# Kernel tuning notes

Hardware: AMD Instinct MI355X
Metric: run time of the kernel (lower is better)

The kernel has to match this reference:

```python
import jax, jax.numpy as jnp
import numpy as np

NUM_NODES = 20000
SEQ_LEN = 128
IN_FEATS = 2
HIDDEN = 32
N_TOTAL = NUM_NODES * SEQ_LEN  # flattened graph size
N_EDGES = 2_000_000


def setup_inputs() -> dict:
    key = jax.random.key(0)
    ks = jax.random.split(key, 10)
    x = jax.random.normal(ks[0], (NUM_NODES, SEQ_LEN, IN_FEATS), dtype=jnp.float32)
    edge_index = jax.random.randint(ks[1], (2, N_EDGES), 0, N_TOTAL, dtype=jnp.int64)
    s = 0.1
    gcn_W = jax.random.normal(ks[2], (IN_FEATS, HIDDEN), dtype=jnp.float32) * s
    gcn_b = jnp.zeros((HIDDEN,), dtype=jnp.float32)
    w_ih = jax.random.normal(ks[3], (4 * HIDDEN, HIDDEN), dtype=jnp.float32) * s
    w_hh = jax.random.normal(ks[4], (4 * HIDDEN, HIDDEN), dtype=jnp.float32) * s
    b_ih = jax.random.normal(ks[5], (4 * HIDDEN,), dtype=jnp.float32) * s
    b_hh = jax.random.normal(ks[6], (4 * HIDDEN,), dtype=jnp.float32) * s
    fc_W = jax.random.normal(ks[7], (HIDDEN, 1), dtype=jnp.float32) * s
    fc_b = jnp.zeros((1,), dtype=jnp.float32)
    return {"x": x, "edge_index": edge_index, "gcn_W": gcn_W, "gcn_b": gcn_b,
            "w_ih": w_ih, "w_hh": w_hh, "b_ih": b_ih, "b_hh": b_hh,
            "fc_W": fc_W, "fc_b": fc_b}


def _gcn(x_flat, edge_index, W, b):
    # PyG GCNConv: add self-loops, symmetric normalization, then linear+bias.
    src, dst = edge_index[0], edge_index[1]
    n = x_flat.shape[0]
    # degree at target side, including the self-loop (+1)
    deg = jax.ops.segment_sum(jnp.ones_like(dst, dtype=x_flat.dtype), dst, num_segments=n) + 1.0
    dinv = jax.lax.rsqrt(deg)  # deg >= 1 always (self-loop)
    h = x_flat @ W  # [n, HIDDEN] transform before propagate
    norm = dinv[src] * dinv[dst]  # [E]
    msg = h[src] * norm[:, None]  # gather + per-edge scale
    agg = jax.ops.segment_sum(msg, dst, num_segments=n)
    # self-loop contribution: dinv_i * dinv_i * h_i = h_i / deg_i
    out = agg + h * (1.0 / deg)[:, None]
    return out + b


def _lstm(xs, w_ih, w_hh, b_ih, b_hh):
    # torch LSTM gate order: i, f, g, o. xs: [N, S, H] -> final hidden [N, H]
    n, s, hdim = xs.shape
    xs_t = jnp.swapaxes(xs, 0, 1)  # [S, N, H]
    # precompute input projections once (dense GEMM)
    x_proj = xs_t @ w_ih.T + b_ih + b_hh  # [S, N, 4H]

    def step(carry, xp):
        h, c = carry
        g = xp + h @ w_hh.T  # [N, 4H]
        i, f, gg, o = jnp.split(g, 4, axis=-1)
        c = jax.nn.sigmoid(f) * c + jax.nn.sigmoid(i) * jnp.tanh(gg)
        h = jax.nn.sigmoid(o) * jnp.tanh(c)
        return (h, c), None

    h0 = jnp.zeros((n, hdim), dtype=xs.dtype)
    (hn, _), _ = jax.lax.scan(step, (h0, h0), x_proj)
    return hn


def reference(x, edge_index, gcn_W, gcn_b, w_ih, w_hh, b_ih, b_hh, fc_W, fc_b):
    num_nodes, seq_len, num_feats = x.shape
    x_in = x.reshape(-1, num_feats)  # [N*S, F]
    x_gcn = jax.nn.relu(_gcn(x_in, edge_index, gcn_W, gcn_b))
    x_lstm = x_gcn.reshape(num_nodes, seq_len, -1)
    hn = _lstm(x_lstm, w_ih, w_hh, b_ih, b_hh)
    return hn @ fc_W + fc_b  # [num_nodes, 1]
```

## Files before the change

kernel.cpp:

```cpp
#include <hip/hip_runtime.h>

#define SEQ 128
#define HID 32
#define TPB 128
#define XS 56

typedef __attribute__((ext_vector_type(8))) short short8;
typedef __attribute__((ext_vector_type(4))) short short4v;
typedef __attribute__((ext_vector_type(4))) float floatx4;


__global__ void count_kernel(const int* __restrict__ idx, int E, int* __restrict__ cnt) {
    int e = (blockIdx.x * blockDim.x + threadIdx.x) * 4;
    if (((E & 3) == 0) && e + 3 < E) {
        int4 d = *(const int4*)(idx + E + e);
        atomicAdd(&cnt[d.x], 1);
        atomicAdd(&cnt[d.y], 1);
        atomicAdd(&cnt[d.z], 1);
        atomicAdd(&cnt[d.w], 1);
    } else {
        int lim = min(e + 4, E);
        for (int k = e; k < lim; ++k) atomicAdd(&cnt[idx[E + k]], 1);
    }
}

__device__ __forceinline__ unsigned long long pk2(float xx, float yy, float dv) {
    int qx = __float2int_rn(xx * dv * 2097152.0f);
    int qy = __float2int_rn(yy * dv * 2097152.0f);
    return ((unsigned long long)(unsigned)(qx + (1 << 26)) << 32) |
           (unsigned)(qy + (1 << 26));
}

__global__ void scatter_pk_kernel(const int* __restrict__ idx, int E,
                                  const float2* __restrict__ x2,
                                  const int* __restrict__ deg,
                                  unsigned long long* __restrict__ aggP) {
    int e = (blockIdx.x * blockDim.x + threadIdx.x) * 4;
    if (((E & 3) == 0) && e + 3 < E) {
        int4 s = *(const int4*)(idx + e);
        int4 d = *(const int4*)(idx + E + e);
        float2 v0 = x2[s.x];
        float2 v1 = x2[s.y];
        float2 v2 = x2[s.z];
        float2 v3 = x2[s.w];
        float dv0 = rsqrtf((float)deg[s.x] + 1.0f);
        float dv1 = rsqrtf((float)deg[s.y] + 1.0f);
        float dv2 = rsqrtf((float)deg[s.z] + 1.0f);
        float dv3 = rsqrtf((float)deg[s.w] + 1.0f);
        atomicAdd(&aggP[d.x], pk2(v0.x, v0.y, dv0));
        atomicAdd(&aggP[d.y], pk2(v1.x, v1.y, dv1));
        atomicAdd(&aggP[d.z], pk2(v2.x, v2.y, dv2));
        atomicAdd(&aggP[d.w], pk2(v3.x, v3.y, dv3));
    } else {
        int lim = min(e + 4, E);
        for (int k = e; k < lim; ++k) {
            int s = idx[k];
            int d = idx[E + k];
            float2 v = x2[s];
            float dv = rsqrtf((float)deg[s] + 1.0f);
            atomicAdd(&aggP[d], pk2(v.x, v.y, dv));
        }
    }
}


__device__ __forceinline__ float sigm_f(float x) {
    return __builtin_amdgcn_rcpf(1.0f + __expf(-x));
}
__device__ __forceinline__ float tanh_f(float x) {
    return fmaf(__builtin_amdgcn_rcpf(1.0f + __expf(-2.0f * x)), 2.0f, -1.0f);
}
__device__ __forceinline__ void fsplit(float f, short& hi, short& lo) {
    unsigned u = __float_as_uint(f);
    hi = (short)(u >> 16);
    float r = f - __uint_as_float(u & 0xFFFF0000u);
    lo = (short)(__float_as_uint(r) >> 16);
}

__global__ __launch_bounds__(TPB, 2) void lstm_mfma4_kernel(
    const float2* __restrict__ x2,
    const unsigned long long* __restrict__ aggP, const int* __restrict__ deg,
    int N,
    const float* __restrict__ gcn_W, const float* __restrict__ gcn_b,
    const float* __restrict__ w_ih, const float* __restrict__ w_hh,
    const float* __restrict__ b_ih, const float* __restrict__ b_hh,
    const float* __restrict__ fc_W, const float* __restrict__ fc_b,
    float* __restrict__ out) {
    __shared__ float2 ubuf[16][SEQ + 1];
    __shared__ __align__(16) short hhb[2][16][XS];
    __shared__ __align__(16) short hlb[2][16][XS];
    __shared__ float fcp[2][16];

    const int tid = threadIdx.x;
    const int w = tid >> 6;
    const int lane = tid & 63;
    const int l15 = lane & 15;
    const int q = lane >> 4;
    const int base = blockIdx.x * 16;

    {
        const float2* xb = x2 + (size_t)base * SEQ;
        const unsigned long long* apb = aggP + (size_t)base * SEQ;
        const int* dgb = deg + (size_t)base * SEQ;
        const int lim = min(16 * SEQ, (N - base) * SEQ);
        for (int i = tid; i < 16 * SEQ; i += TPB) {
            float2 v = make_float2(0.f, 0.f);
            if (i < lim) {
                int dg = dgb[i];
                float dv = rsqrtf((float)dg + 1.0f);
                float2 xx = xb[i];
                unsigned long long pk = apb[i];
                unsigned bias = (unsigned)dg * 67108864u;
                float ax = (float)((int)((unsigned)(pk >> 32) - bias)) * (1.0f / 2097152.0f);
                float ay = (float)((int)((unsigned)pk - bias)) * (1.0f / 2097152.0f);
                v = make_float2(dv * fmaf(xx.x, dv, ax), dv * fmaf(xx.y, dv, ay));
            }
            ubuf[i >> 7][i & 127] = v;
        }
        if (tid < 16) ubuf[tid][SEQ] = make_float2(0.f, 0.f);
    }

    short8 AiH[4], AiL[4], AhH[4], AhL[4];
    floatx4 biasC[4];
    #pragma unroll
    for (int g = 0; g < 4; ++g) {
        const int arow = g * 32 + 8 * (l15 >> 2) + 4 * w + (l15 & 3);
        const float* wi = w_ih + arow * HID + 8 * q;
        const float* wh = w_hh + arow * HID + 8 * q;
        #pragma unroll
        for (int j = 0; j < 8; ++j) {
            short h16, l16;
            fsplit(wi[j], h16, l16); AiH[g][j] = h16; AiL[g][j] = l16;
            fsplit(wh[j], h16, l16); AhH[g][j] = h16; AhL[g][j] = l16;
        }
        #pragma unroll
        for (int r = 0; r < 4; ++r) {
            const int brow = g * 32 + 8 * q + 4 * w + r;
            biasC[g][r] = b_ih[brow] + b_hh[brow];
        }
    }

    float wg0[8], wg1[8], gbc[8];
    #pragma unroll
    for (int j = 0; j < 8; ++j) {
        const int u = 8 * q + j;
        wg0[j] = gcn_W[u];
        wg1[j] = gcn_W[HID + u];
        gbc[j] = gcn_b[u];
    }
    float fcw[4];
    #pragma unroll
    for (int r = 0; r < 4; ++r) fcw[r] = fc_W[8 * q + 4 * w + r];

    float c[4] = {0.f, 0.f, 0.f, 0.f};
    float ho[4] = {0.f, 0.f, 0.f, 0.f};

    __syncthreads();

#define XG_FRAGS(TT, XH, XL)                                                  \
    {                                                                         \
        float2 uu = ubuf[l15][TT];                                            \
        _Pragma("unroll") for (int j = 0; j < 8; ++j) {                       \
            float g = fmaxf(fmaf(uu.x, wg0[j], fmaf(uu.y, wg1[j], gbc[j])), 0.f); \
            short h16, l16;                                                   \
            fsplit(g, h16, l16);                                              \
            XH[j] = h16; XL[j] = l16;                                         \
        }                                                                     \
    }

    *(short4v*)&hhb[0][l15][8 * q + 4 * w] = (short4v){0, 0, 0, 0};
    *(short4v*)&hlb[0][l15][8 * q + 4 * w] = (short4v){0, 0, 0, 0};
    short8 xhA, xlA, xhB, xlB;
    floatx4 aXA[4], aXB[4];
    XG_FRAGS(0, xhA, xlA);
    #pragma unroll
    for (int g = 0; g < 4; ++g)
        aXA[g] = __builtin_amdgcn_mfma_f32_16x16x32_bf16(AiH[g], xhA, biasC[g], 0, 0, 0);
    #pragma unroll
    for (int g = 0; g < 4; ++g)
        aXA[g] = __builtin_amdgcn_mfma_f32_16x16x32_bf16(AiL[g], xhA, aXA[g], 0, 0, 0);
    #pragma unroll
    for (int g = 0; g < 4; ++g)
        aXA[g] = __builtin_amdgcn_mfma_f32_16x16x32_bf16(AiH[g], xlA, aXA[g], 0, 0, 0);
    __syncthreads();

#define LSTM_STEP(P, TT, AXC, AXN, XHN, XLN)                                               \
    do {                                                                                   \
        const short8 hh = *(const short8*)&hhb[P][l15][8 * q];                             \
        const short8 hl = *(const short8*)&hlb[P][l15][8 * q];                             \
        floatx4 acc[4];                                                                    \
        __builtin_amdgcn_s_setprio(1);                                                     \
        _Pragma("unroll") for (int g = 0; g < 4; ++g)                                      \
            acc[g] = __builtin_amdgcn_mfma_f32_16x16x32_bf16(AhH[g], hh, AXC[g], 0, 0, 0); \
        _Pragma("unroll") for (int g = 0; g < 4; ++g)                                      \
            acc[g] = __builtin_amdgcn_mfma_f32_16x16x32_bf16(AhL[g], hh, acc[g], 0, 0, 0); \
        _Pragma("unroll") for (int g = 0; g < 4; ++g)                                      \
            acc[g] = __builtin_amdgcn_mfma_f32_16x16x32_bf16(AhH[g], hl, acc[g], 0, 0, 0); \
        __builtin_amdgcn_s_setprio(0);                                                     \
        XG_FRAGS((TT) + 1, XHN, XLN);                                                      \
        __builtin_amdgcn_s_setprio(1);                                                     \
        _Pragma("unroll") for (int g = 0; g < 4; ++g)                                      \
            AXN[g] = __builtin_amdgcn_mfma_f32_16x16x32_bf16(AiH[g], XHN, biasC[g], 0, 0, 0); \
        _Pragma("unroll") for (int g = 0; g < 4; ++g)                                      \
            AXN[g] = __builtin_amdgcn_mfma_f32_16x16x32_bf16(AiL[g], XHN, AXN[g], 0, 0, 0); \
        _Pragma("unroll") for (int g = 0; g < 4; ++g)                                      \
            AXN[g] = __builtin_amdgcn_mfma_f32_16x16x32_bf16(AiH[g], XLN, AXN[g], 0, 0, 0); \
        __builtin_amdgcn_s_setprio(0);                                                     \
        {                                                                                  \
            short hi[4], lo[4];                                                            \
            _Pragma("unroll") for (int r = 0; r < 4; ++r) {                                \
                const float ig = sigm_f(acc[0][r]);                                        \
                const float fg = sigm_f(acc[1][r]);                                        \
                const float gg = tanh_f(acc[2][r]);                                        \
                const float og = sigm_f(acc[3][r]);                                        \
                c[r] = fmaf(fg, c[r], ig * gg);                                            \
                const float hv = og * tanh_f(c[r]);                                        \
                ho[r] = hv;                                                                \
                fsplit(hv, hi[r], lo[r]);                                                  \
            }                                                                              \
            *(short4v*)&hhb[(P) ^ 1][l15][8 * q + 4 * w] =                                 \
                (short4v){hi[0], hi[1], hi[2], hi[3]};                                     \
            *(short4v*)&hlb[(P) ^ 1][l15][8 * q + 4 * w] =                                 \
                (short4v){lo[0], lo[1], lo[2], lo[3]};                                     \
        }                                                                                  \
        __syncthreads();                                                                   \
    } while (0)

    #pragma unroll 1
    for (int t = 0; t < SEQ; t += 2) {
        LSTM_STEP(0, t,     aXA, aXB, xhB, xlB);
        LSTM_STEP(1, t + 1, aXB, aXA, xhA, xlA);
    }
#undef LSTM_STEP
#undef XG_FRAGS

    float partial = fmaf(ho[0], fcw[0], fmaf(ho[1], fcw[1],
                    fmaf(ho[2], fcw[2], ho[3] * fcw[3])));
    partial += __shfl_xor(partial, 16);
    partial += __shfl_xor(partial, 32);
    if (lane < 16) fcp[w][l15] = partial;
    __syncthreads();
    if (w == 0 && lane < 16) {
        const int node = base + l15;
        if (node < N) out[node] = fcp[0][l15] + fcp[1][l15] + fc_b[0];
    }
}

extern "C" void kernel_launch(void* const* d_in, const int* in_sizes, int n_in,
                              void* d_out, int out_size, void* d_ws, size_t ws_size,
                              hipStream_t stream) {
    const float* x     = (const float*)d_in[0];
    const int*   idx   = (const int*)d_in[1];
    const float* gcn_W = (const float*)d_in[2];
    const float* gcn_b = (const float*)d_in[3];
    const float* w_ih  = (const float*)d_in[4];
    const float* w_hh  = (const float*)d_in[5];
    const float* b_ih  = (const float*)d_in[6];
    const float* b_hh  = (const float*)d_in[7];
    const float* fc_W  = (const float*)d_in[8];
    const float* fc_b  = (const float*)d_in[9];

    const int num_nodes = in_sizes[0] / (SEQ * 2);
    const int ntot = num_nodes * SEQ;
    const int E = in_sizes[1] / 2;

    int* deg = (int*)d_ws;
    unsigned long long* aggP = (unsigned long long*)((char*)d_ws + (size_t)ntot * 4);

    hipMemsetAsync(d_ws, 0, (size_t)ntot * 12, stream);

    const int eb = (E + 1023) / 1024;
    count_kernel<<<eb, 256, 0, stream>>>(idx, E, deg);
    scatter_pk_kernel<<<eb, 256, 0, stream>>>(idx, E, (const float2*)x, deg, aggP);
    lstm_mfma4_kernel<<<(num_nodes + 15) / 16, TPB, 0, stream>>>(
        (const float2*)x, aggP, deg, num_nodes,
        gcn_W, gcn_b, w_ih, w_hh, b_ih, b_hh, fc_W, fc_b,
        (float*)d_out);
}
```

Before: 489.5 us.

## Run each LSTM 16-node tile in one wavefront with register-resident hidden state

The LSTM kernel moves from two waves per 16-node tile to a single 64-lane wave that computes all 32 hidden units. Weight rows are permuted so the MFMA accumulator layout matches the B-operand layout, which lets the new hidden state feed the next step straight from registers. This removes the per-timestep LDS write/read of h and the block barrier. In exchange each wave holds twice the weight fragments and accumulators and issues twice the MFMAs serially, which raises register pressure and lengthens the per-wave dependency chain.

```diff
diff --git a/kernel.cpp b/kernel.cpp
--- a/kernel.cpp
+++ b/kernel.cpp
@@ -2,11 +2,8 @@
 
 #define SEQ 128
 #define HID 32
-#define TPB 128
-#define XS 56
 
 typedef __attribute__((ext_vector_type(8))) short short8;
-typedef __attribute__((ext_vector_type(4))) short short4v;
 typedef __attribute__((ext_vector_type(4))) float floatx4;
 
 
@@ -77,7 +74,7 @@
     lo = (short)(__float_as_uint(r) >> 16);
 }
 
-__global__ __launch_bounds__(TPB, 2) void lstm_mfma4_kernel(
+__global__ __launch_bounds__(64, 1) void lstm_sw_kernel(
     const float2* __restrict__ x2,
     const unsigned long long* __restrict__ aggP, const int* __restrict__ deg,
     int N,
@@ -87,15 +84,10 @@
     const float* __restrict__ fc_W, const float* __restrict__ fc_b,
     float* __restrict__ out) {
     __shared__ float2 ubuf[16][SEQ + 1];
-    __shared__ __align__(16) short hhb[2][16][XS];
-    __shared__ __align__(16) short hlb[2][16][XS];
-    __shared__ float fcp[2][16];
-
-    const int tid = threadIdx.x;
-    const int w = tid >> 6;
-    const int lane = tid & 63;
-    const int l15 = lane & 15;
-    const int q = lane >> 4;
+
+    const int lane = threadIdx.x;
+    const int n = lane & 15;
+    const int qq = lane >> 4;
     const int base = blockIdx.x * 16;
 
     {
@@ -103,7 +95,8 @@
         const unsigned long long* apb = aggP + (size_t)base * SEQ;
         const int* dgb = deg + (size_t)base * SEQ;
         const int lim = min(16 * SEQ, (N - base) * SEQ);
-        for (int i = tid; i < 16 * SEQ; i += TPB) {
+        #pragma unroll 4
+        for (int i = lane; i < 16 * SEQ; i += 64) {
             float2 v = make_float2(0.f, 0.f);
             if (i < lim) {
                 int dg = dgb[i];
@@ -117,132 +110,154 @@
             }
             ubuf[i >> 7][i & 127] = v;
         }
-        if (tid < 16) ubuf[tid][SEQ] = make_float2(0.f, 0.f);
-    }
-
-    short8 AiH[4], AiL[4], AhH[4], AhL[4];
-    floatx4 biasC[4];
+        if (lane < 16) ubuf[lane][SEQ] = make_float2(0.f, 0.f);
+    }
+
+    short8 AiH[4][2], AiL[4][2], AhH[4][2], AhL[4][2];
+    floatx4 biasC[4][2];
     #pragma unroll
     for (int g = 0; g < 4; ++g) {
-        const int arow = g * 32 + 8 * (l15 >> 2) + 4 * w + (l15 & 3);
-        const float* wi = w_ih + arow * HID + 8 * q;
-        const float* wh = w_hh + arow * HID + 8 * q;
-        #pragma unroll
-        for (int j = 0; j < 8; ++j) {
-            short h16, l16;
-            fsplit(wi[j], h16, l16); AiH[g][j] = h16; AiL[g][j] = l16;
-            fsplit(wh[j], h16, l16); AhH[g][j] = h16; AhL[g][j] = l16;
-        }
-        #pragma unroll
-        for (int r = 0; r < 4; ++r) {
-            const int brow = g * 32 + 8 * q + 4 * w + r;
-            biasC[g][r] = b_ih[brow] + b_hh[brow];
-        }
-    }
-
-    float wg0[8], wg1[8], gbc[8];
+        #pragma unroll
+        for (int t1 = 0; t1 < 2; ++t1) {
+            const int arow = g * 32 + 8 * (n >> 2) + 4 * t1 + (n & 3);
+            const float* wi = w_ih + arow * HID + 8 * qq;
+            const float* wh = w_hh + arow * HID + 8 * qq;
+            #pragma unroll
+            for (int j = 0; j < 8; ++j) {
+                short h16, l16;
+                fsplit(wi[j], h16, l16); AiH[g][t1][j] = h16; AiL[g][t1][j] = l16;
+                fsplit(wh[j], h16, l16); AhH[g][t1][j] = h16; AhL[g][t1][j] = l16;
+            }
+            #pragma unroll
+            for (int r = 0; r < 4; ++r) {
+                const int brow = g * 32 + 8 * qq + 4 * t1 + r;
+                biasC[g][t1][r] = b_ih[brow] + b_hh[brow];
+            }
+        }
+    }
+
+    float wg0[8], wg1[8], gbc[8], fcw[8];
     #pragma unroll
     for (int j = 0; j < 8; ++j) {
-        const int u = 8 * q + j;
+        const int u = 8 * qq + j;
         wg0[j] = gcn_W[u];
         wg1[j] = gcn_W[HID + u];
         gbc[j] = gcn_b[u];
-    }
-    float fcw[4];
-    #pragma unroll
-    for (int r = 0; r < 4; ++r) fcw[r] = fc_W[8 * q + 4 * w + r];
-
-    float c[4] = {0.f, 0.f, 0.f, 0.f};
-    float ho[4] = {0.f, 0.f, 0.f, 0.f};
-
-    __syncthreads();
-
-#define XG_FRAGS(TT, XH, XL)                                                  \
-    {                                                                         \
-        float2 uu = ubuf[l15][TT];                                            \
-        _Pragma("unroll") for (int j = 0; j < 8; ++j) {                       \
-            float g = fmaxf(fmaf(uu.x, wg0[j], fmaf(uu.y, wg1[j], gbc[j])), 0.f); \
-            short h16, l16;                                                   \
-            fsplit(g, h16, l16);                                              \
-            XH[j] = h16; XL[j] = l16;                                         \
-        }                                                                     \
-    }
-
-    *(short4v*)&hhb[0][l15][8 * q + 4 * w] = (short4v){0, 0, 0, 0};
-    *(short4v*)&hlb[0][l15][8 * q + 4 * w] = (short4v){0, 0, 0, 0};
-    short8 xhA, xlA, xhB, xlB;
-    floatx4 aXA[4], aXB[4];
-    XG_FRAGS(0, xhA, xlA);
+        fcw[j] = fc_W[u];
+    }
+
+    float c[2][4], ho[2][4];
+    #pragma unroll
+    for (int t1 = 0; t1 < 2; ++t1)
+        #pragma unroll
+        for (int r = 0; r < 4; ++r) { c[t1][r] = 0.f; ho[t1][r] = 0.f; }
+
+    short8 hh = (short8){0, 0, 0, 0, 0, 0, 0, 0};
+    short8 hl = (short8){0, 0, 0, 0, 0, 0, 0, 0};
+    short8 xh, xl;
+    floatx4 aX[4][2];
+
+    {
+        float2 uu = ubuf[n][0];
+        #pragma unroll
+        for (int j = 0; j < 8; ++j) {
+            float g = fmaxf(fmaf(uu.x, wg0[j], fmaf(uu.y, wg1[j], gbc[j])), 0.f);
+            short h16, l16;
+            fsplit(g, h16, l16);
+            xh[j] = h16; xl[j] = l16;
+        }
+    }
     #pragma unroll
     for (int g = 0; g < 4; ++g)
-        aXA[g] = __builtin_amdgcn_mfma_f32_16x16x32_bf16(AiH[g], xhA, biasC[g], 0, 0, 0);
+        #pragma unroll
+        for (int t1 = 0; t1 < 2; ++t1)
+            aX[g][t1] = __builtin_amdgcn_mfma_f32_16x16x32_bf16(AiH[g][t1], xh, biasC[g][t1], 0, 0, 0);
     #pragma unroll
     for (int g = 0; g < 4; ++g)
-        aXA[g] = __builtin_amdgcn_mfma_f32_16x16x32_bf16(AiL[g], xhA, aXA[g], 0, 0, 0);
+        #pragma unroll
+        for (int t1 = 0; t1 < 2; ++t1)
+            aX[g][t1] = __builtin_amdgcn_mfma_f32_16x16x32_bf16(AiL[g][t1], xh, aX[g][t1], 0, 0, 0);
     #pragma unroll
     for (int g = 0; g < 4; ++g)
-        aXA[g] = __builtin_amdgcn_mfma_f32_16x16x32_bf16(AiH[g], xlA, aXA[g], 0, 0, 0);
-    __syncthreads();
-
-#define LSTM_STEP(P, TT, AXC, AXN, XHN, XLN)                                               \
-    do {                                                                                   \
-        const short8 hh = *(const short8*)&hhb[P][l15][8 * q];                             \
-        const short8 hl = *(const short8*)&hlb[P][l15][8 * q];                             \
-        floatx4 acc[4];                                                                    \
-        __builtin_amdgcn_s_setprio(1);                                                     \
-        _Pragma("unroll") for (int g = 0; g < 4; ++g)                                      \
-            acc[g] = __builtin_amdgcn_mfma_f32_16x16x32_bf16(AhH[g], hh, AXC[g], 0, 0, 0); \
-        _Pragma("unroll") for (int g = 0; g < 4; ++g)                                      \
-            acc[g] = __builtin_amdgcn_mfma_f32_16x16x32_bf16(AhL[g], hh, acc[g], 0, 0, 0); \
-        _Pragma("unroll") for (int g = 0; g < 4; ++g)                                      \
-            acc[g] = __builtin_amdgcn_mfma_f32_16x16x32_bf16(AhH[g], hl, acc[g], 0, 0, 0); \
-        __builtin_amdgcn_s_setprio(0);                                                     \
-        XG_FRAGS((TT) + 1, XHN, XLN);                                                      \
-        __builtin_amdgcn_s_setprio(1);                                                     \
-        _Pragma("unroll") for (int g = 0; g < 4; ++g)                                      \
-            AXN[g] = __builtin_amdgcn_mfma_f32_16x16x32_bf16(AiH[g], XHN, biasC[g], 0, 0, 0); \
-        _Pragma("unroll") for (int g = 0; g < 4; ++g)                                      \
-            AXN[g] = __builtin_amdgcn_mfma_f32_16x16x32_bf16(AiL[g], XHN, AXN[g], 0, 0, 0); \
-        _Pragma("unroll") for (int g = 0; g < 4; ++g)                                      \
-            AXN[g] = __builtin_amdgcn_mfma_f32_16x16x32_bf16(AiH[g], XLN, AXN[g], 0, 0, 0); \
-        __builtin_amdgcn_s_setprio(0);                                                     \
-        {                                                                                  \
-            short hi[4], lo[4];                                                            \
-            _Pragma("unroll") for (int r = 0; r < 4; ++r) {                                \
-                const float ig = sigm_f(acc[0][r]);                                        \
-                const float fg = sigm_f(acc[1][r]);                                        \
-                const float gg = tanh_f(acc[2][r]);                                        \
-                const float og = sigm_f(acc[3][r]);                                        \
-                c[r] = fmaf(fg, c[r], ig * gg);                                            \
-                const float hv = og * tanh_f(c[r]);                                        \
-                ho[r] = hv;                                                                \
-                fsplit(hv, hi[r], lo[r]);                                                  \
-            }                                                                              \
-            *(short4v*)&hhb[(P) ^ 1][l15][8 * q + 4 * w] =                                 \
-                (short4v){hi[0], hi[1], hi[2], hi[3]};                                     \
-            *(short4v*)&hlb[(P) ^ 1][l15][8 * q + 4 * w] =                                 \
-                (short4v){lo[0], lo[1], lo[2], lo[3]};                                     \
-        }                                                                                  \
-        __syncthreads();                                                                   \
-    } while (0)
+        #pragma unroll
+        for (int t1 = 0; t1 < 2; ++t1)
+            aX[g][t1] = __builtin_amdgcn_mfma_f32_16x16x32_bf16(AiH[g][t1], xl, aX[g][t1], 0, 0, 0);
 
     #pragma unroll 1
-    for (int t = 0; t < SEQ; t += 2) {
-        LSTM_STEP(0, t,     aXA, aXB, xhB, xlB);
-        LSTM_STEP(1, t + 1, aXB, aXA, xhA, xlA);
-    }
-#undef LSTM_STEP
-#undef XG_FRAGS
-
-    float partial = fmaf(ho[0], fcw[0], fmaf(ho[1], fcw[1],
-                    fmaf(ho[2], fcw[2], ho[3] * fcw[3])));
+    for (int t = 0; t < SEQ; ++t) {
+        floatx4 acc[4][2];
+        #pragma unroll
+        for (int g = 0; g < 4; ++g)
+            #pragma unroll
+            for (int t1 = 0; t1 < 2; ++t1)
+                acc[g][t1] = __builtin_amdgcn_mfma_f32_16x16x32_bf16(AhH[g][t1], hh, aX[g][t1], 0, 0, 0);
+        #pragma unroll
+        for (int g = 0; g < 4; ++g)
+            #pragma unroll
+            for (int t1 = 0; t1 < 2; ++t1)
+                acc[g][t1] = __builtin_amdgcn_mfma_f32_16x16x32_bf16(AhL[g][t1], hh, acc[g][t1], 0, 0, 0);
+        #pragma unroll
+        for (int g = 0; g < 4; ++g)
+            #pragma unroll
+            for (int t1 = 0; t1 < 2; ++t1)
+                acc[g][t1] = __builtin_amdgcn_mfma_f32_16x16x32_bf16(AhH[g][t1], hl, acc[g][t1], 0, 0, 0);
+
+        {
+            float2 uu = ubuf[n][t + 1];
+            #pragma unroll
+            for (int j = 0; j < 8; ++j) {
+                float g = fmaxf(fmaf(uu.x, wg0[j], fmaf(uu.y, wg1[j], gbc[j])), 0.f);
+                short h16, l16;
+                fsplit(g, h16, l16);
+                xh[j] = h16; xl[j] = l16;
+            }
+        }
+        #pragma unroll
+        for (int g = 0; g < 4; ++g)
+            #pragma unroll
+            for (int t1 = 0; t1 < 2; ++t1)
+                aX[g][t1] = __builtin_amdgcn_mfma_f32_16x16x32_bf16(AiH[g][t1], xh, biasC[g][t1], 0, 0, 0);
+        #pragma unroll
+        for (int g = 0; g < 4; ++g)
+            #pragma unroll
+            for (int t1 = 0; t1 < 2; ++t1)
+                aX[g][t1] = __builtin_amdgcn_mfma_f32_16x16x32_bf16(AiL[g][t1], xh, aX[g][t1], 0, 0, 0);
+        #pragma unroll
+        for (int g = 0; g < 4; ++g)
+            #pragma unroll
+            for (int t1 = 0; t1 < 2; ++t1)
+                aX[g][t1] = __builtin_amdgcn_mfma_f32_16x16x32_bf16(AiH[g][t1], xl, aX[g][t1], 0, 0, 0);
+
+        #pragma unroll
+        for (int t1 = 0; t1 < 2; ++t1) {
+            #pragma unroll
+            for (int r = 0; r < 4; ++r) {
+                const float ig = sigm_f(acc[0][t1][r]);
+                const float fg = sigm_f(acc[1][t1][r]);
+                const float gg = tanh_f(acc[2][t1][r]);
+                const float og = sigm_f(acc[3][t1][r]);
+                c[t1][r] = fmaf(fg, c[t1][r], ig * gg);
+                const float hv = og * tanh_f(c[t1][r]);
+                ho[t1][r] = hv;
+                short h16, l16;
+                fsplit(hv, h16, l16);
+                hh[4 * t1 + r] = h16;
+                hl[4 * t1 + r] = l16;
+            }
+        }
+    }
+
+    float partial = 0.f;
+    #pragma unroll
+    for (int t1 = 0; t1 < 2; ++t1)
+        #pragma unroll
+        for (int r = 0; r < 4; ++r)
+            partial = fmaf(ho[t1][r], fcw[4 * t1 + r], partial);
     partial += __shfl_xor(partial, 16);
     partial += __shfl_xor(partial, 32);
-    if (lane < 16) fcp[w][l15] = partial;
-    __syncthreads();
-    if (w == 0 && lane < 16) {
-        const int node = base + l15;
-        if (node < N) out[node] = fcp[0][l15] + fcp[1][l15] + fc_b[0];
+    if (lane < 16) {
+        const int node = base + n;
+        if (node < N) out[node] = partial + fc_b[0];
     }
 }
 
@@ -272,7 +287,7 @@
     const int eb = (E + 1023) / 1024;
     count_kernel<<<eb, 256, 0, stream>>>(idx, E, deg);
     scatter_pk_kernel<<<eb, 256, 0, stream>>>(idx, E, (const float2*)x, deg, aggP);
-    lstm_mfma4_kernel<<<(num_nodes + 15) / 16, TPB, 0, stream>>>(
+    lstm_sw_kernel<<<(num_nodes + 15) / 16, 64, 0, stream>>>(
         (const float2*)x, aggP, deg, num_nodes,
         gcn_W, gcn_b, w_ih, w_hh, b_ih, b_hh, fc_W, fc_b,
         (float*)d_out);
```

Measured after the change: 542.3 us. 10.8% more time.

## Swap MFMA operand roles in LSTM kernel and fold gate scaling into weights

Applied to the files above, without the earlier changes.

Restructures the LSTM recurrence so activations become the A operand and weights the B operand. Each lane now owns one gate row across four nodes, and the input projection is computed inside the same step instead of being software-pipelined one step ahead. The log2(e) factor (doubled for the g gate) is folded into the weights and bias, so the sigmoids can use raw exp2. The hidden state is written back element-wise into a narrower shared buffer, launch bounds rise to 3 blocks per SM, and the input fragments are packed with perm instructions. In exchange, the input-projection MFMAs now sit on the serial dependency chain and shared-memory stores become scalar.

```diff
diff --git a/kernel.cpp b/kernel.cpp
--- a/kernel.cpp
+++ b/kernel.cpp
@@ -2,11 +2,10 @@
 
 #define SEQ 128
 #define HID 32
-#define TPB 128
-#define XS 56
+#define TPB2 128
+#define XS 40
 
 typedef __attribute__((ext_vector_type(8))) short short8;
-typedef __attribute__((ext_vector_type(4))) short short4v;
 typedef __attribute__((ext_vector_type(4))) float floatx4;
 
 
@@ -64,8 +63,8 @@
 }
 
 
-__device__ __forceinline__ float sigm_f(float x) {
-    return __builtin_amdgcn_rcpf(1.0f + __expf(-x));
+__device__ __forceinline__ float sg(float y) {
+    return __builtin_amdgcn_rcpf(1.0f + __builtin_amdgcn_exp2f(-y));
 }
 __device__ __forceinline__ float tanh_f(float x) {
     return fmaf(__builtin_amdgcn_rcpf(1.0f + __expf(-2.0f * x)), 2.0f, -1.0f);
@@ -76,8 +75,16 @@
     float r = f - __uint_as_float(u & 0xFFFF0000u);
     lo = (short)(__float_as_uint(r) >> 16);
 }
-
-__global__ __launch_bounds__(TPB, 2) void lstm_mfma4_kernel(
+__device__ __forceinline__ void fsplit2(float a, float b, unsigned& hi, unsigned& lo) {
+    unsigned ta = __float_as_uint(a) & 0xFFFF0000u;
+    unsigned tb = __float_as_uint(b) & 0xFFFF0000u;
+    float ra = a - __uint_as_float(ta);
+    float rb = b - __uint_as_float(tb);
+    hi = __builtin_amdgcn_perm(__float_as_uint(b), __float_as_uint(a), 0x07060302u);
+    lo = __builtin_amdgcn_perm(__float_as_uint(rb), __float_as_uint(ra), 0x07060302u);
+}
+
+__global__ __launch_bounds__(TPB2, 3) void lstm_sw2_kernel(
     const float2* __restrict__ x2,
     const unsigned long long* __restrict__ aggP, const int* __restrict__ deg,
     int N,
@@ -92,9 +99,9 @@
     __shared__ float fcp[2][16];
 
     const int tid = threadIdx.x;
-    const int w = tid >> 6;
+    const int t1 = tid >> 6;
     const int lane = tid & 63;
-    const int l15 = lane & 15;
+    const int n = lane & 15;
     const int q = lane >> 4;
     const int base = blockIdx.x * 16;
 
@@ -103,7 +110,7 @@
         const unsigned long long* apb = aggP + (size_t)base * SEQ;
         const int* dgb = deg + (size_t)base * SEQ;
         const int lim = min(16 * SEQ, (N - base) * SEQ);
-        for (int i = tid; i < 16 * SEQ; i += TPB) {
+        for (int i = tid; i < 16 * SEQ; i += TPB2) {
             float2 v = make_float2(0.f, 0.f);
             if (i < lim) {
                 int dg = dgb[i];
@@ -118,26 +125,28 @@
             ubuf[i >> 7][i & 127] = v;
         }
         if (tid < 16) ubuf[tid][SEQ] = make_float2(0.f, 0.f);
-    }
-
-    short8 AiH[4], AiL[4], AhH[4], AhL[4];
-    floatx4 biasC[4];
+        for (int i = tid; i < 320; i += TPB2) {
+            ((int*)hhb[0])[i] = 0;
+            ((int*)hlb[0])[i] = 0;
+        }
+    }
+
+    short8 WiH[4], WiL[4], WhH[4], WhL[4];
+    floatx4 biasv[4];
     #pragma unroll
     for (int g = 0; g < 4; ++g) {
-        const int arow = g * 32 + 8 * (l15 >> 2) + 4 * w + (l15 & 3);
+        const float gsc = (g == 2) ? 2.8853900817779268f : 1.4426950408889634f;
+        const int arow = g * 32 + 16 * t1 + n;
         const float* wi = w_ih + arow * HID + 8 * q;
         const float* wh = w_hh + arow * HID + 8 * q;
         #pragma unroll
         for (int j = 0; j < 8; ++j) {
             short h16, l16;
-            fsplit(wi[j], h16, l16); AiH[g][j] = h16; AiL[g][j] = l16;
-            fsplit(wh[j], h16, l16); AhH[g][j] = h16; AhL[g][j] = l16;
-        }
-        #pragma unroll
-        for (int r = 0; r < 4; ++r) {
-            const int brow = g * 32 + 8 * q + 4 * w + r;
-            biasC[g][r] = b_ih[brow] + b_hh[brow];
-        }
+            fsplit(wi[j] * gsc, h16, l16); WiH[g][j] = h16; WiL[g][j] = l16;
+            fsplit(wh[j] * gsc, h16, l16); WhH[g][j] = h16; WhL[g][j] = l16;
+        }
+        const float bb = (b_ih[arow] + b_hh[arow]) * gsc;
+        biasv[g] = (floatx4){bb, bb, bb, bb};
     }
 
     float wg0[8], wg1[8], gbc[8];
@@ -148,101 +157,94 @@
         wg1[j] = gcn_W[HID + u];
         gbc[j] = gcn_b[u];
     }
-    float fcw[4];
-    #pragma unroll
-    for (int r = 0; r < 4; ++r) fcw[r] = fc_W[8 * q + 4 * w + r];
+    const float fcw = fc_W[16 * t1 + n];
 
     float c[4] = {0.f, 0.f, 0.f, 0.f};
     float ho[4] = {0.f, 0.f, 0.f, 0.f};
 
+#define XG_FRAGS(TT, XH, XL)                                                      \
+    {                                                                             \
+        float2 uu = ubuf[n][TT];                                                  \
+        float gv[8];                                                              \
+        _Pragma("unroll") for (int j = 0; j < 8; ++j)                             \
+            gv[j] = fmaxf(fmaf(uu.x, wg0[j], fmaf(uu.y, wg1[j], gbc[j])), 0.f);   \
+        unsigned hp0, lp0, hp1, lp1, hp2, lp2, hp3, lp3;                          \
+        fsplit2(gv[0], gv[1], hp0, lp0);                                          \
+        fsplit2(gv[2], gv[3], hp1, lp1);                                          \
+        fsplit2(gv[4], gv[5], hp2, lp2);                                          \
+        fsplit2(gv[6], gv[7], hp3, lp3);                                          \
+        int4 th = make_int4((int)hp0, (int)hp1, (int)hp2, (int)hp3);              \
+        int4 tl = make_int4((int)lp0, (int)lp1, (int)lp2, (int)lp3);              \
+        XH = *(short8*)&th;                                                       \
+        XL = *(short8*)&tl;                                                       \
+    }
+
+    short8 xh, xl;
+    XG_FRAGS(0, xh, xl);
     __syncthreads();
 
-#define XG_FRAGS(TT, XH, XL)                                                  \
-    {                                                                         \
-        float2 uu = ubuf[l15][TT];                                            \
-        _Pragma("unroll") for (int j = 0; j < 8; ++j) {                       \
-            float g = fmaxf(fmaf(uu.x, wg0[j], fmaf(uu.y, wg1[j], gbc[j])), 0.f); \
-            short h16, l16;                                                   \
-            fsplit(g, h16, l16);                                              \
-            XH[j] = h16; XL[j] = l16;                                         \
-        }                                                                     \
-    }
-
-    *(short4v*)&hhb[0][l15][8 * q + 4 * w] = (short4v){0, 0, 0, 0};
-    *(short4v*)&hlb[0][l15][8 * q + 4 * w] = (short4v){0, 0, 0, 0};
-    short8 xhA, xlA, xhB, xlB;
-    floatx4 aXA[4], aXB[4];
-    XG_FRAGS(0, xhA, xlA);
-    #pragma unroll
-    for (int g = 0; g < 4; ++g)
-        aXA[g] = __builtin_amdgcn_mfma_f32_16x16x32_bf16(AiH[g], xhA, biasC[g], 0, 0, 0);
-    #pragma unroll
-    for (int g = 0; g < 4; ++g)
-        aXA[g] = __builtin_amdgcn_mfma_f32_16x16x32_bf16(AiL[g], xhA, aXA[g], 0, 0, 0);
-    #pragma unroll
-    for (int g = 0; g < 4; ++g)
-        aXA[g] = __builtin_amdgcn_mfma_f32_16x16x32_bf16(AiH[g], xlA, aXA[g], 0, 0, 0);
-    __syncthreads();
-
-#define LSTM_STEP(P, TT, AXC, AXN, XHN, XLN)                                               \
-    do {                                                                                   \
-        const short8 hh = *(const short8*)&hhb[P][l15][8 * q];                             \
-        const short8 hl = *(const short8*)&hlb[P][l15][8 * q];                             \
-        floatx4 acc[4];                                                                    \
-        __builtin_amdgcn_s_setprio(1);                                                     \
-        _Pragma("unroll") for (int g = 0; g < 4; ++g)                                      \
-            acc[g] = __builtin_amdgcn_mfma_f32_16x16x32_bf16(AhH[g], hh, AXC[g], 0, 0, 0); \
-        _Pragma("unroll") for (int g = 0; g < 4; ++g)                                      \
-            acc[g] = __builtin_amdgcn_mfma_f32_16x16x32_bf16(AhL[g], hh, acc[g], 0, 0, 0); \
-        _Pragma("unroll") for (int g = 0; g < 4; ++g)                                      \
-            acc[g] = __builtin_amdgcn_mfma_f32_16x16x32_bf16(AhH[g], hl, acc[g], 0, 0, 0); \
-        __builtin_amdgcn_s_setprio(0);                                                     \
-        XG_FRAGS((TT) + 1, XHN, XLN);                                                      \
-        __builtin_amdgcn_s_setprio(1);                                                     \
-        _Pragma("unroll") for (int g = 0; g < 4; ++g)                                      \
-            AXN[g] = __builtin_amdgcn_mfma_f32_16x16x32_bf16(AiH[g], XHN, biasC[g], 0, 0, 0); \
-        _Pragma("unroll") for (int g = 0; g < 4; ++g)                                      \
-            AXN[g] = __builtin_amdgcn_mfma_f32_16x16x32_bf16(AiL[g], XHN, AXN[g], 0, 0, 0); \
-        _Pragma("unroll") for (int g = 0; g < 4; ++g)                                      \
-            AXN[g] = __builtin_amdgcn_mfma_f32_16x16x32_bf16(AiH[g], XLN, AXN[g], 0, 0, 0); \
-        __builtin_amdgcn_s_setprio(0);                                                     \
-        {                                                                                  \
-            short hi[4], lo[4];                                                            \
-            _Pragma("unroll") for (int r = 0; r < 4; ++r) {                                \
-                const float ig = sigm_f(acc[0][r]);                                        \
-                const float fg = sigm_f(acc[1][r]);                                        \
-                const float gg = tanh_f(acc[2][r]);                                        \
-                const float og = sigm_f(acc[3][r]);                                        \
-                c[r] = fmaf(fg, c[r], ig * gg);                                            \
-                const float hv = og * tanh_f(c[r]);                                        \
-                ho[r] = hv;                                                                \
-                fsplit(hv, hi[r], lo[r]);                                                  \
-            }                                                                              \
-            *(short4v*)&hhb[(P) ^ 1][l15][8 * q + 4 * w] =                                 \
-                (short4v){hi[0], hi[1], hi[2], hi[3]};                                     \
-            *(short4v*)&hlb[(P) ^ 1][l15][8 * q + 4 * w] =                                 \
-                (short4v){lo[0], lo[1], lo[2], lo[3]};                                     \
-        }                                                                                  \
-        __syncthreads();                                                                   \
+#define LSTM_STEP(P, TT)                                                                    \
+    do {                                                                                    \
+        const short8 hh = *(const short8*)&hhb[P][n][8 * q];                                \
+        const short8 hl = *(const short8*)&hlb[P][n][8 * q];                                \
+        floatx4 acc[4];                                                                     \
+        __builtin_amdgcn_s_setprio(1);                                                      \
+        _Pragma("unroll") for (int g = 0; g < 4; ++g)                                       \
+            acc[g] = __builtin_amdgcn_mfma_f32_16x16x32_bf16(xh, WiH[g], biasv[g], 0, 0, 0); \
+        _Pragma("unroll") for (int g = 0; g < 4; ++g)                                       \
+            acc[g] = __builtin_amdgcn_mfma_f32_16x16x32_bf16(xh, WiL[g], acc[g], 0, 0, 0);  \
+        _Pragma("unroll") for (int g = 0; g < 4; ++g)                                       \
+            acc[g] = __builtin_amdgcn_mfma_f32_16x16x32_bf16(xl, WiH[g], acc[g], 0, 0, 0);  \
+        _Pragma("unroll") for (int g = 0; g < 4; ++g)                                       \
+            acc[g] = __builtin_amdgcn_mfma_f32_16x16x32_bf16(hh, WhH[g], acc[g], 0, 0, 0);  \
+        _Pragma("unroll") for (int g = 0; g < 4; ++g)                                       \
+            acc[g] = __builtin_amdgcn_mfma_f32_16x16x32_bf16(hh, WhL[g], acc[g], 0, 0, 0);  \
+        _Pragma("unroll") for (int g = 0; g < 4; ++g)                                       \
+            acc[g] = __builtin_amdgcn_mfma_f32_16x16x32_bf16(hl, WhH[g], acc[g], 0, 0, 0);  \
+        __builtin_amdgcn_s_setprio(0);                                                      \
+        XG_FRAGS((TT) + 1, xh, xl);              \
+        _Pragma("unroll") for (int r = 0; r < 4; ++r) {                                     \
+            const float ig = sg(acc[0][r]);                                                 \
+            const float fg = sg(acc[1][r]);                                                 \
+            const float gg = fmaf(sg(acc[2][r]), 2.0f, -1.0f);                              \
+            const float og = sg(acc[3][r]);                                                 \
+            c[r] = fmaf(fg, c[r], ig * gg);                                                 \
+            const float hv = og * tanh_f(c[r]);                                             \
+            ho[r] = hv;                                                                     \
+            short h16, l16;                                                                 \
+            fsplit(hv, h16, l16);                                                           \
+            hhb[(P) ^ 1][4 * q + r][16 * t1 + n] = h16;                                     \
+            hlb[(P) ^ 1][4 * q + r][16 * t1 + n] = l16;                                     \
+        }                                                                                   \
+        __syncthreads();                                                                    \
     } while (0)
 
     #pragma unroll 1
     for (int t = 0; t < SEQ; t += 2) {
-        LSTM_STEP(0, t,     aXA, aXB, xhB, xlB);
-        LSTM_STEP(1, t + 1, aXB, aXA, xhA, xlA);
+        LSTM_STEP(0, t);
+        LSTM_STEP(1, t + 1);
     }
 #undef LSTM_STEP
 #undef XG_FRAGS
 
-    float partial = fmaf(ho[0], fcw[0], fmaf(ho[1], fcw[1],
-                    fmaf(ho[2], fcw[2], ho[3] * fcw[3])));
-    partial += __shfl_xor(partial, 16);
-    partial += __shfl_xor(partial, 32);
-    if (lane < 16) fcp[w][l15] = partial;
+    float p0 = ho[0] * fcw, p1 = ho[1] * fcw, p2 = ho[2] * fcw, p3 = ho[3] * fcw;
+    #pragma unroll
+    for (int m = 1; m < 16; m <<= 1) {
+        p0 += __shfl_xor(p0, m);
+        p1 += __shfl_xor(p1, m);
+        p2 += __shfl_xor(p2, m);
+        p3 += __shfl_xor(p3, m);
+    }
+    if (n == 0) {
+        fcp[t1][4 * q + 0] = p0;
+        fcp[t1][4 * q + 1] = p1;
+        fcp[t1][4 * q + 2] = p2;
+        fcp[t1][4 * q + 3] = p3;
+    }
     __syncthreads();
-    if (w == 0 && lane < 16) {
-        const int node = base + l15;
-        if (node < N) out[node] = fcp[0][l15] + fcp[1][l15] + fc_b[0];
+    if (t1 == 0 && lane < 16) {
+        const int node = base + lane;
+        if (node < N) out[node] = fcp[0][lane] + fcp[1][lane] + fc_b[0];
     }
 }
 
@@ -272,7 +274,7 @@
     const int eb = (E + 1023) / 1024;
     count_kernel<<<eb, 256, 0, stream>>>(idx, E, deg);
     scatter_pk_kernel<<<eb, 256, 0, stream>>>(idx, E, (const float2*)x, deg, aggP);
-    lstm_mfma4_kernel<<<(num_nodes + 15) / 16, TPB, 0, stream>>>(
+    lstm_sw2_kernel<<<(num_nodes + 15) / 16, TPB2, 0, stream>>>(
         (const float2*)x, aggP, deg, num_nodes,
         gcn_W, gcn_b, w_ih, w_hh, b_ih, b_hh, fc_W, fc_b,
         (float*)d_out);
```

Result: faster. 471.6 us (-3.7%).
